# Kernel optimization log

Hardware: AMD Instinct MI355X
Metric: run time of the kernel (lower is better)

The kernel has to match this reference:

```python
import jax, jax.numpy as jnp
import numpy as np

ROPE_BASE = 100.0  # CroCo RoPE2D default freq


def _rope1d(tok, pos):
    # tok: [B, H, N, D], pos: [B, N] int
    D = tok.shape[-1]
    inv_freq = 1.0 / (ROPE_BASE ** (jnp.arange(0, D, 2, dtype=jnp.float32) / D))
    ang = pos[..., None].astype(jnp.float32) * inv_freq          # [B, N, D/2]
    cos = jnp.concatenate([jnp.cos(ang), jnp.cos(ang)], -1)[:, None]  # [B,1,N,D]
    sin = jnp.concatenate([jnp.sin(ang), jnp.sin(ang)], -1)[:, None]
    x1, x2 = jnp.split(tok, 2, axis=-1)
    rot = jnp.concatenate([-x2, x1], -1)
    return tok * cos.astype(tok.dtype) + rot * sin.astype(tok.dtype)


def _rope2d(tok, pos):
    # first half of head channels rotated with y coords, second half with x
    t_y, t_x = jnp.split(tok, 2, axis=-1)
    return jnp.concatenate([_rope1d(t_y, pos[..., 0]), _rope1d(t_x, pos[..., 1])], -1)


def setup_inputs() -> dict:
    key0 = jax.random.key(0)
    ks = jax.random.split(key0, 10)
    B, Nq, Nk, C, H = 4, 2048, 2048, 1024, 16
    s = 1.0 / np.sqrt(C)
    return {
        "query": jax.random.normal(ks[0], (B, Nq, C), jnp.float32),
        "key": jax.random.normal(ks[1], (B, Nk, C), jnp.float32),
        "value": jax.random.normal(ks[2], (B, Nk, C), jnp.float32),
        "qpos": jax.random.randint(ks[3], (B, Nq, 2), 0, 64),
        "kpos": jax.random.randint(ks[4], (B, Nk, 2), 0, 64),
        "Wq": jax.random.normal(ks[5], (C, C), jnp.float32) * s,
        "Wk": jax.random.normal(ks[6], (C, C), jnp.float32) * s,
        "Wv": jax.random.normal(ks[7], (C, C), jnp.float32) * s,
        "Wo": jax.random.normal(ks[8], (C, C), jnp.float32) * s,
        "bo": jax.random.normal(ks[9], (C,), jnp.float32) * 0.01,
    }


def reference(query, key, value, qpos, kpos, Wq, Wk, Wv, Wo, bo):
    B, Nq, C = query.shape
    H = 16
    D = C // H
    scale = D ** (-0.5)
    # separate Q/K/V projections (torch Linear: x @ W.T), split into heads
    q = (query @ Wq.T).reshape(B, Nq, H, D).transpose(0, 2, 1, 3)
    k = (key @ Wk.T).reshape(B, key.shape[1], H, D).transpose(0, 2, 1, 3)
    v = (value @ Wv.T).reshape(B, value.shape[1], H, D).transpose(0, 2, 1, 3)
    # inline fp16 cast around RoPE, as in the original
    q = _rope2d(q.astype(jnp.float16), qpos).astype(jnp.float32)
    k = _rope2d(k.astype(jnp.float16), kpos).astype(jnp.float32)
    # SDPA
    scores = jnp.einsum("bhqd,bhkd->bhqk", q, k) * scale
    attn = jax.nn.softmax(scores, axis=-1)
    x = jnp.einsum("bhqk,bhkd->bhqd", attn, v)
    x = x.transpose(0, 2, 1, 3).reshape(B, Nq, C)
    return x @ Wo.T + bo
```

## Files before the change

kernel.cpp:

```cpp
#include <hip/hip_runtime.h>
#include <math.h>

typedef _Float16 half_t;
typedef __attribute__((ext_vector_type(8))) _Float16 f16x8;
typedef __attribute__((ext_vector_type(4))) _Float16 f16x4;
typedef __attribute__((ext_vector_type(4))) float f32x4;

#define MFMA16(a, b, c) __builtin_amdgcn_mfma_f32_16x16x32_f16((a), (b), (c), 0, 0, 0)

constexpr int Bc = 4, NQ = 2048, NKC = 2048, CC = 1024, NHD = 16, HDIM = 64;

__device__ __forceinline__ void async_copy16(half_t* lds, const half_t* g) {
  __builtin_amdgcn_global_load_lds(
      (const __attribute__((address_space(1))) unsigned*)g,
      (__attribute__((address_space(3))) unsigned*)lds, 16, 0, 0);
}

__global__ __launch_bounds__(256) void cvt16(const float* __restrict__ src,
                                             half_t* __restrict__ dst) {
  const int i = blockIdx.x * 256 + threadIdx.x;
  const f32x4 a = ((const f32x4*)src)[2 * i];
  const f32x4 b = ((const f32x4*)src)[2 * i + 1];
  f16x8 h;
#pragma unroll
  for (int j = 0; j < 4; ++j) { h[j] = (half_t)a[j]; h[4 + j] = (half_t)b[j]; }
  ((f16x8*)dst)[i] = h;
}

__global__ __launch_bounds__(256) void cvtW(const float* __restrict__ s0,
                                            const float* __restrict__ s1,
                                            const float* __restrict__ s2,
                                            const float* __restrict__ s3,
                                            half_t* __restrict__ dst) {
  const int y = blockIdx.y;
  const float* src = (y == 0) ? s0 : (y == 1) ? s1 : (y == 2) ? s2 : s3;
  const int i = blockIdx.x * 256 + threadIdx.x;
  const f32x4 a = ((const f32x4*)src)[2 * i];
  const f32x4 b = ((const f32x4*)src)[2 * i + 1];
  f16x8 h;
#pragma unroll
  for (int j = 0; j < 4; ++j) { h[j] = (half_t)a[j]; h[4 + j] = (half_t)b[j]; }
  ((f16x8*)(dst + (size_t)y * CC * CC))[i] = h;
}

template <bool FINAL>
__global__ __launch_bounds__(256) void gemm_lds(const half_t* __restrict__ X,
                                                const half_t* __restrict__ W,
                                                half_t* __restrict__ out16,
                                                float* __restrict__ outf,
                                                const float* __restrict__ bias) {
  __shared__ half_t As[128 * 32];
  __shared__ half_t Bs[128 * 32];
  const int tid  = threadIdx.x;
  const int wave = tid >> 6, lane = tid & 63;
  const int quad = lane >> 4, l16 = lane & 15;
  const int m0 = blockIdx.y * 128, n0 = blockIdx.x * 128;
  const int mw = (wave >> 1) * 64, nw = (wave & 1) * 64;

  const int srow = lane >> 2, skoff = (lane & 3) * 8;
  const half_t* xa = X + (size_t)(m0 + wave * 32 + srow) * CC + skoff;
  const half_t* xb = W + (size_t)(n0 + wave * 32 + srow) * CC + skoff;
  half_t* lA0 = &As[(wave * 2 + 0) * 512];
  half_t* lA1 = &As[(wave * 2 + 1) * 512];
  half_t* lB0 = &Bs[(wave * 2 + 0) * 512];
  half_t* lB1 = &Bs[(wave * 2 + 1) * 512];

  f32x4 acc[4][4] = {};

  for (int k0 = 0; k0 < CC; k0 += 32) {
    __syncthreads();
    async_copy16(lA0, xa + k0);
    async_copy16(lA1, xa + 16 * CC + k0);
    async_copy16(lB0, xb + k0);
    async_copy16(lB1, xb + 16 * CC + k0);
    __syncthreads();

    f16x8 af[4], bf[4];
#pragma unroll
    for (int mi = 0; mi < 4; ++mi) af[mi] = *(const f16x8*)&As[(mw + mi * 16 + l16) * 32 + quad * 8];
#pragma unroll
    for (int ni = 0; ni < 4; ++ni) bf[ni] = *(const f16x8*)&Bs[(nw + ni * 16 + l16) * 32 + quad * 8];
#pragma unroll
    for (int mi = 0; mi < 4; ++mi)
#pragma unroll
      for (int ni = 0; ni < 4; ++ni) acc[mi][ni] = MFMA16(af[mi], bf[ni], acc[mi][ni]);
  }

#pragma unroll
  for (int mi = 0; mi < 4; ++mi)
#pragma unroll
    for (int ni = 0; ni < 4; ++ni)
#pragma unroll
      for (int r = 0; r < 4; ++r) {
        const size_t row = (size_t)(m0 + mw + mi * 16 + quad * 4 + r);
        const size_t col = (size_t)(n0 + nw + ni * 16 + l16);
        if constexpr (FINAL) outf[row * CC + col] = acc[mi][ni][r] + bias[col];
        else                 out16[row * CC + col] = (half_t)acc[mi][ni][r];
      }
}

__global__ __launch_bounds__(256) void rope_kernel(half_t* __restrict__ t,
                                                   const int* __restrict__ pos) {
#pragma clang fp contract(off)
  const int gid = blockIdx.x * 256 + threadIdx.x;
  const int i       = gid & 15;
  const int halfsel = (gid >> 4) & 1;
  const int h       = (gid >> 5) & 15;
  const int n       = (gid >> 9) & 2047;
  const int b       = gid >> 20;

  const int p = pos[((b * NQ + n) << 1) + halfsel];
  const float inv = __builtin_amdgcn_exp2f((float)i * -0.41524100904865773f);
  const float ang = (float)p * inv;
  const half_t hc = (half_t)cosf(ang);
  const half_t hs = (half_t)sinf(ang);

  const size_t base = (size_t)(b * NQ + n) * CC + h * HDIM + halfsel * 32;
  const half_t t1 = t[base + i];
  const half_t t2 = t[base + 16 + i];
  const half_t p1 = t1 * hc;
  const half_t p2 = t2 * hs;
  const half_t p3 = t2 * hc;
  const half_t p4 = t1 * hs;
  t[base + i]      = p1 - p2;
  t[base + 16 + i] = p3 + p4;
}

__global__ __launch_bounds__(256, 4) void attn_kernel(const half_t* __restrict__ q16,
                                                      const half_t* __restrict__ k16,
                                                      const half_t* __restrict__ v16,
                                                      half_t* __restrict__ x16) {
  __shared__ __align__(16) half_t Kf[2 * 4096];
  __shared__ __align__(16) unsigned Vfd[2 * 4 * 64 * 4];
  __shared__ __align__(16) unsigned Pb[4][2][16][32];

  const int tid  = threadIdx.x;
  const int wave = tid >> 6, lane = tid & 63;
  const int quad = lane >> 4, l16 = lane & 15;
  const int lx   = lane ^ quad;
  const int psw  = (l16 & 7) << 2;
  const int qblk = blockIdx.x, h = blockIdx.y, b = blockIdx.z;
  const f32x4 zero = {0.f, 0.f, 0.f, 0.f};

  f16x8 qa[2][2];
  {
    const half_t* qbase =
        q16 + (size_t)(b * NQ + qblk * 128 + wave * 32 + l16) * CC + h * HDIM + quad * 8;
#pragma unroll
    for (int mi = 0; mi < 2; ++mi)
#pragma unroll
      for (int kc = 0; kc < 2; ++kc)
        qa[mi][kc] = *(const f16x8*)(qbase + (size_t)mi * 16 * CC + kc * 32);
  }

  f32x4 o[2][4] = {};
  f32x4 lpv[2] = {};

  const half_t* kga = k16 + (size_t)(b * NKC + wave * 16 + l16) * CC + h * HDIM + quad * 8;

  const int vp = tid & 31, vd0 = (tid >> 5) * 8;
  const half_t* vptr = v16 + (size_t)(b * NKC + 2 * vp) * CC + h * HDIM + vd0;
  const int vkc = vp >> 4, vqd = (vp & 15) >> 2, vnd = vd0 >> 4;
  const int vl16b = vd0 & 15;
  const int vswz  = vqd ^ (vkc << 2);
  const int vbase = ((vkc * 4 + vnd) * 64 + vqd * 16) * 4 + (vp & 3);

  async_copy16(&Kf[(wave * 2 + 0) * 512], kga);
  async_copy16(&Kf[(wave * 2 + 1) * 512], kga + 32);
  f16x8 vr0 = *(const f16x8*)vptr;
  f16x8 vr1 = *(const f16x8*)(vptr + CC);

  int cur = 0;
  for (int kt = 0; kt < NKC; kt += 64) {
#pragma unroll
    for (int i = 0; i < 8; ++i) {
      union { half_t h2[2]; unsigned u; } pk;
      pk.h2[0] = vr0[i]; pk.h2[1] = vr1[i];
      Vfd[vbase + (((vl16b + i) ^ vswz) << 2)] = pk.u;
    }
    __syncthreads();

    if (kt + 64 < NKC) {
      const half_t* kn = kga + (size_t)(kt + 64) * CC;
      async_copy16(&Kf[(cur ^ 1) * 4096 + (wave * 2 + 0) * 512], kn);
      async_copy16(&Kf[(cur ^ 1) * 4096 + (wave * 2 + 1) * 512], kn + 32);
      const half_t* vn = vptr + (size_t)(kt + 64) * CC;
      vr0 = *(const f16x8*)vn;
      vr1 = *(const f16x8*)(vn + CC);
    }

    const half_t* Kc = &Kf[cur * 4096];

    f32x4 st[2][4];
    __builtin_amdgcn_s_setprio(1);
#pragma unroll
    for (int kb = 0; kb < 4; ++kb) {
      const f16x8 ka0 = *(const f16x8*)&Kc[((kb * 2 + 0) * 64 + lane) * 8];
      const f16x8 ka1 = *(const f16x8*)&Kc[((kb * 2 + 1) * 64 + lane) * 8];
#pragma unroll
      for (int mi = 0; mi < 2; ++mi) {
        const f32x4 t0 = MFMA16(ka0, qa[mi][0], zero);
        st[mi][kb] = MFMA16(ka1, qa[mi][1], t0);
      }
    }
    __builtin_amdgcn_s_setprio(0);

#pragma unroll
    for (int mi = 0; mi < 2; ++mi)
#pragma unroll
      for (int kb = 0; kb < 4; ++kb) {
        f16x4 w;
#pragma unroll
        for (int r = 0; r < 4; ++r) {
          const float p = __builtin_amdgcn_exp2f(st[mi][kb][r] * 0.18033688011112042f);
          lpv[mi][r] += p;
          w[r] = (half_t)p;
        }
        *(f16x4*)&Pb[wave][mi][l16][(kb * 8 + quad * 2) ^ psw] = w;
      }

    __builtin_amdgcn_s_setprio(1);
#pragma unroll
    for (int kc = 0; kc < 2; ++kc) {
      const f16x8 pa0 = *(const f16x8*)&Pb[wave][0][l16][(kc * 16 + quad * 4) ^ psw];
      const f16x8 pa1 = *(const f16x8*)&Pb[wave][1][l16][(kc * 16 + quad * 4) ^ psw];
#pragma unroll
      for (int nd = 0; nd < 4; ++nd) {
        const f16x8 vb = *(const f16x8*)&Vfd[(((kc * 4 + nd) * 64) + (lx ^ (kc << 2))) * 4];
        o[0][nd] = MFMA16(vb, pa0, o[0][nd]);
        o[1][nd] = MFMA16(vb, pa1, o[1][nd]);
      }
    }
    __builtin_amdgcn_s_setprio(0);

    asm volatile("s_waitcnt lgkmcnt(0)" ::: "memory");
    __builtin_amdgcn_s_barrier();
    cur ^= 1;
  }

#pragma unroll
  for (int mi = 0; mi < 2; ++mi) {
    float rs = (lpv[mi][0] + lpv[mi][1]) + (lpv[mi][2] + lpv[mi][3]);
    rs += __shfl_xor(rs, 16);
    rs += __shfl_xor(rs, 32);
    const float inv = 1.f / rs;
    const size_t row =
        (size_t)(b * NQ + qblk * 128 + wave * 32 + mi * 16 + l16) * CC + h * HDIM;
#pragma unroll
    for (int nd = 0; nd < 4; ++nd) {
      f16x4 w;
#pragma unroll
      for (int r = 0; r < 4; ++r) w[r] = (half_t)(o[mi][nd][r] * inv);
      *(f16x4*)&x16[row + nd * 16 + quad * 4] = w;
    }
  }
}

extern "C" void kernel_launch(void* const* d_in, const int* in_sizes, int n_in,
                              void* d_out, int out_size, void* d_ws, size_t ws_size,
                              hipStream_t stream) {
  const float* query = (const float*)d_in[0];
  const float* key   = (const float*)d_in[1];
  const float* value = (const float*)d_in[2];
  const int*   qpos  = (const int*)d_in[3];
  const int*   kpos  = (const int*)d_in[4];
  const float* Wq = (const float*)d_in[5];
  const float* Wk = (const float*)d_in[6];
  const float* Wv = (const float*)d_in[7];
  const float* Wo = (const float*)d_in[8];
  const float* bo = (const float*)d_in[9];
  float* out = (float*)d_out;

  const size_t NT = (size_t)Bc * NQ * CC;
  half_t* q16 = (half_t*)d_ws;
  half_t* k16 = q16 + NT;
  half_t* v16 = k16 + NT;
  half_t* A0  = v16 + NT;
  half_t* W16 = A0 + NT;
  half_t* x16 = A0;

  const int nbA = (int)(NT / 8 / 256);
  const int nbW = (CC * CC) / 8 / 256;

  cvtW<<<dim3(nbW, 4), 256, 0, stream>>>(Wq, Wk, Wv, Wo, W16);

  const dim3 gg(CC / 128, Bc * NQ / 128);
  cvt16<<<nbA, 256, 0, stream>>>(query, A0);
  gemm_lds<false><<<gg, 256, 0, stream>>>(A0, W16 + 0 * (size_t)CC * CC, q16, nullptr, nullptr);
  cvt16<<<nbA, 256, 0, stream>>>(key, A0);
  gemm_lds<false><<<gg, 256, 0, stream>>>(A0, W16 + 1 * (size_t)CC * CC, k16, nullptr, nullptr);
  cvt16<<<nbA, 256, 0, stream>>>(value, A0);
  gemm_lds<false><<<gg, 256, 0, stream>>>(A0, W16 + 2 * (size_t)CC * CC, v16, nullptr, nullptr);

  rope_kernel<<<(Bc * NQ * NHD * 32) / 256, 256, 0, stream>>>(q16, qpos);
  rope_kernel<<<(Bc * NQ * NHD * 32) / 256, 256, 0, stream>>>(k16, kpos);

  attn_kernel<<<dim3(NQ / 128, NHD, Bc), 256, 0, stream>>>(q16, k16, v16, x16);

  gemm_lds<true><<<gg, 256, 0, stream>>>(x16, W16 + 3 * (size_t)CC * CC, nullptr, out, bo);
}
```

Before: 405.0 us.

## Fuse fp32-to-fp16 input conversion and RoPE into projection GEMMs

The projection GEMMs now read fp32 activations directly, convert them to fp16 in registers and store them to LDS, prefetching the next k-slice into registers. The q and k GEMM epilogues apply RoPE inline before writing fp16 output. This drops three cvt16 launches and two rope launches, along with the fp16 staging traffic they caused. In exchange the A tile goes through a synchronous register-to-LDS path, and the epilogue recomputes sin/cos per element.

After: 969.9 us. +139.5%, slower.

```diff
diff --git a/kernel.cpp b/kernel.cpp
--- a/kernel.cpp
+++ b/kernel.cpp
@@ -14,17 +14,6 @@
   __builtin_amdgcn_global_load_lds(
       (const __attribute__((address_space(1))) unsigned*)g,
       (__attribute__((address_space(3))) unsigned*)lds, 16, 0, 0);
-}
-
-__global__ __launch_bounds__(256) void cvt16(const float* __restrict__ src,
-                                             half_t* __restrict__ dst) {
-  const int i = blockIdx.x * 256 + threadIdx.x;
-  const f32x4 a = ((const f32x4*)src)[2 * i];
-  const f32x4 b = ((const f32x4*)src)[2 * i + 1];
-  f16x8 h;
-#pragma unroll
-  for (int j = 0; j < 4; ++j) { h[j] = (half_t)a[j]; h[4 + j] = (half_t)b[j]; }
-  ((f16x8*)dst)[i] = h;
 }
 
 __global__ __launch_bounds__(256) void cvtW(const float* __restrict__ s0,
@@ -43,12 +32,13 @@
   ((f16x8*)(dst + (size_t)y * CC * CC))[i] = h;
 }
 
-template <bool FINAL>
-__global__ __launch_bounds__(256) void gemm_lds(const half_t* __restrict__ X,
-                                                const half_t* __restrict__ W,
-                                                half_t* __restrict__ out16,
-                                                float* __restrict__ outf,
-                                                const float* __restrict__ bias) {
+template <bool CVT, bool ROPE, bool FINAL>
+__global__ __launch_bounds__(256) void gemm_k(const void* __restrict__ Xv,
+                                              const half_t* __restrict__ W,
+                                              half_t* __restrict__ out16,
+                                              float* __restrict__ outf,
+                                              const float* __restrict__ bias,
+                                              const int* __restrict__ pos) {
   __shared__ half_t As[128 * 32];
   __shared__ half_t Bs[128 * 32];
   const int tid  = threadIdx.x;
@@ -58,23 +48,52 @@
   const int mw = (wave >> 1) * 64, nw = (wave & 1) * 64;
 
   const int srow = lane >> 2, skoff = (lane & 3) * 8;
-  const half_t* xa = X + (size_t)(m0 + wave * 32 + srow) * CC + skoff;
   const half_t* xb = W + (size_t)(n0 + wave * 32 + srow) * CC + skoff;
+  half_t* lB0 = &Bs[(wave * 2 + 0) * 512];
+  half_t* lB1 = &Bs[(wave * 2 + 1) * 512];
+
+  const half_t* xa = CVT ? nullptr : (const half_t*)Xv + (size_t)(m0 + wave * 32 + srow) * CC + skoff;
   half_t* lA0 = &As[(wave * 2 + 0) * 512];
   half_t* lA1 = &As[(wave * 2 + 1) * 512];
-  half_t* lB0 = &Bs[(wave * 2 + 0) * 512];
-  half_t* lB1 = &Bs[(wave * 2 + 1) * 512];
+
+  const int arow = tid >> 1, akh = (tid & 1) * 16;
+  const float* xsrc = CVT ? (const float*)Xv + (size_t)(m0 + arow) * CC + akh : nullptr;
+  half_t* adst = &As[arow * 32 + akh];
 
   f32x4 acc[4][4] = {};
+  f32x4 ar[4];
+  if constexpr (CVT) {
+#pragma unroll
+    for (int j = 0; j < 4; ++j) ar[j] = ((const f32x4*)xsrc)[j];
+  }
 
   for (int k0 = 0; k0 < CC; k0 += 32) {
     __syncthreads();
-    async_copy16(lA0, xa + k0);
-    async_copy16(lA1, xa + 16 * CC + k0);
+    if constexpr (CVT) {
+      f16x8 h0, h1;
+#pragma unroll
+      for (int j = 0; j < 4; ++j) {
+        h0[j] = (half_t)ar[0][j]; h0[4 + j] = (half_t)ar[1][j];
+        h1[j] = (half_t)ar[2][j]; h1[4 + j] = (half_t)ar[3][j];
+      }
+      *(f16x8*)adst = h0;
+      *(f16x8*)(adst + 8) = h1;
+    } else {
+      async_copy16(lA0, xa + k0);
+      async_copy16(lA1, xa + 16 * CC + k0);
+    }
     async_copy16(lB0, xb + k0);
     async_copy16(lB1, xb + 16 * CC + k0);
     __syncthreads();
 
+    if constexpr (CVT) {
+      if (k0 + 32 < CC) {
+        const float* xn = xsrc + k0 + 32;
+#pragma unroll
+        for (int j = 0; j < 4; ++j) ar[j] = ((const f32x4*)xn)[j];
+      }
+    }
+
     f16x8 af[4], bf[4];
 #pragma unroll
     for (int mi = 0; mi < 4; ++mi) af[mi] = *(const f16x8*)&As[(mw + mi * 16 + l16) * 32 + quad * 8];
@@ -86,44 +105,54 @@
       for (int ni = 0; ni < 4; ++ni) acc[mi][ni] = MFMA16(af[mi], bf[ni], acc[mi][ni]);
   }
 
-#pragma unroll
-  for (int mi = 0; mi < 4; ++mi)
-#pragma unroll
-    for (int ni = 0; ni < 4; ++ni)
-#pragma unroll
-      for (int r = 0; r < 4; ++r) {
-        const size_t row = (size_t)(m0 + mw + mi * 16 + quad * 4 + r);
-        const size_t col = (size_t)(n0 + nw + ni * 16 + l16);
-        if constexpr (FINAL) outf[row * CC + col] = acc[mi][ni][r] + bias[col];
-        else                 out16[row * CC + col] = (half_t)acc[mi][ni][r];
-      }
-}
-
-__global__ __launch_bounds__(256) void rope_kernel(half_t* __restrict__ t,
-                                                   const int* __restrict__ pos) {
+  if constexpr (FINAL) {
+#pragma unroll
+    for (int mi = 0; mi < 4; ++mi)
+#pragma unroll
+      for (int ni = 0; ni < 4; ++ni)
+#pragma unroll
+        for (int r = 0; r < 4; ++r) {
+          const size_t row = (size_t)(m0 + mw + mi * 16 + quad * 4 + r);
+          const size_t col = (size_t)(n0 + nw + ni * 16 + l16);
+          outf[row * CC + col] = acc[mi][ni][r] + bias[col];
+        }
+  } else if constexpr (ROPE) {
 #pragma clang fp contract(off)
-  const int gid = blockIdx.x * 256 + threadIdx.x;
-  const int i       = gid & 15;
-  const int halfsel = (gid >> 4) & 1;
-  const int h       = (gid >> 5) & 15;
-  const int n       = (gid >> 9) & 2047;
-  const int b       = gid >> 20;
-
-  const int p = pos[((b * NQ + n) << 1) + halfsel];
-  const float inv = __builtin_amdgcn_exp2f((float)i * -0.41524100904865773f);
-  const float ang = (float)p * inv;
-  const half_t hc = (half_t)cosf(ang);
-  const half_t hs = (half_t)sinf(ang);
-
-  const size_t base = (size_t)(b * NQ + n) * CC + h * HDIM + halfsel * 32;
-  const half_t t1 = t[base + i];
-  const half_t t2 = t[base + 16 + i];
-  const half_t p1 = t1 * hc;
-  const half_t p2 = t2 * hs;
-  const half_t p3 = t2 * hc;
-  const half_t p4 = t1 * hs;
-  t[base + i]      = p1 - p2;
-  t[base + 16 + i] = p3 + p4;
+    const float inv = __builtin_amdgcn_exp2f((float)l16 * -0.41524100904865773f);
+#pragma unroll
+    for (int mi = 0; mi < 4; ++mi)
+#pragma unroll
+      for (int np = 0; np < 2; ++np)
+#pragma unroll
+        for (int r = 0; r < 4; ++r) {
+          const int row = m0 + mw + mi * 16 + quad * 4 + r;
+          const int col1 = n0 + nw + np * 32 + l16;
+          const int halfsel = (col1 >> 5) & 1;
+          const int p = pos[(row << 1) + halfsel];
+          const float ang = (float)p * inv;
+          const half_t hc = (half_t)cosf(ang);
+          const half_t hs = (half_t)sinf(ang);
+          const half_t t1 = (half_t)acc[mi][2 * np + 0][r];
+          const half_t t2 = (half_t)acc[mi][2 * np + 1][r];
+          const half_t p1 = t1 * hc;
+          const half_t p2 = t2 * hs;
+          const half_t p3 = t2 * hc;
+          const half_t p4 = t1 * hs;
+          out16[(size_t)row * CC + col1]      = p1 - p2;
+          out16[(size_t)row * CC + col1 + 16] = p3 + p4;
+        }
+  } else {
+#pragma unroll
+    for (int mi = 0; mi < 4; ++mi)
+#pragma unroll
+      for (int ni = 0; ni < 4; ++ni)
+#pragma unroll
+        for (int r = 0; r < 4; ++r) {
+          const size_t row = (size_t)(m0 + mw + mi * 16 + quad * 4 + r);
+          const size_t col = (size_t)(n0 + nw + ni * 16 + l16);
+          out16[row * CC + col] = (half_t)acc[mi][ni][r];
+        }
+  }
 }
 
 __global__ __launch_bounds__(256, 4) void attn_kernel(const half_t* __restrict__ q16,
@@ -275,27 +304,23 @@
   half_t* q16 = (half_t*)d_ws;
   half_t* k16 = q16 + NT;
   half_t* v16 = k16 + NT;
-  half_t* A0  = v16 + NT;
-  half_t* W16 = A0 + NT;
-  half_t* x16 = A0;
-
-  const int nbA = (int)(NT / 8 / 256);
+  half_t* x16 = v16 + NT;
+  half_t* W16 = x16 + NT;
+
   const int nbW = (CC * CC) / 8 / 256;
 
   cvtW<<<dim3(nbW, 4), 256, 0, stream>>>(Wq, Wk, Wv, Wo, W16);
 
   const dim3 gg(CC / 128, Bc * NQ / 128);
-  cvt16<<<nbA, 256, 0, stream>>>(query, A0);
-  gemm_lds<false><<<gg, 256, 0, stream>>>(A0, W16 + 0 * (size_t)CC * CC, q16, nullptr, nullptr);
-  cvt16<<<nbA, 256, 0, stream>>>(key, A0);
-  gemm_lds<false><<<gg, 256, 0, stream>>>(A0, W16 + 1 * (size_t)CC * CC, k16, nullptr, nullptr);
-  cvt16<<<nbA, 256, 0, stream>>>(value, A0);
-  gemm_lds<false><<<gg, 256, 0, stream>>>(A0, W16 + 2 * (size_t)CC * CC, v16, nullptr, nullptr);
-
-  rope_kernel<<<(Bc * NQ * NHD * 32) / 256, 256, 0, stream>>>(q16, qpos);
-  rope_kernel<<<(Bc * NQ * NHD * 32) / 256, 256, 0, stream>>>(k16, kpos);
+  gemm_k<true, true, false><<<gg, 256, 0, stream>>>(
+      query, W16 + 0 * (size_t)CC * CC, q16, nullptr, nullptr, qpos);
+  gemm_k<true, true, false><<<gg, 256, 0, stream>>>(
+      key, W16 + 1 * (size_t)CC * CC, k16, nullptr, nullptr, kpos);
+  gemm_k<true, false, false><<<gg, 256, 0, stream>>>(
+      value, W16 + 2 * (size_t)CC * CC, v16, nullptr, nullptr, nullptr);
 
   attn_kernel<<<dim3(NQ / 128, NHD, Bc), 256, 0, stream>>>(q16, k16, v16, x16);
 
-  gemm_lds<true><<<gg, 256, 0, stream>>>(x16, W16 + 3 * (size_t)CC * CC, nullptr, out, bo);
-}
+  gemm_k<false, false, true><<<gg, 256, 0, stream>>>(
+      x16, W16 + 3 * (size_t)CC * CC, nullptr, out, bo, nullptr);
+}
```
